# Kernel optimization log

Hardware: AMD Instinct MI355X
Metric: run time of the kernel (lower is better)

## Reference

```python
import jax, jax.numpy as jnp
import numpy as np

B, S, H, L, NH, OUT = 64, 512, 512, 2, 8, 1
HD = H // NH
SKIP_INTERVAL = 2
EPS = 1e-5


def ln(x, g, b):
    m = x.mean(-1, keepdims=True)
    v = x.var(-1, keepdims=True)
    return (x - m) / jnp.sqrt(v + EPS) * g + b


def setup_inputs() -> dict:
    key = jax.random.key(0)
    ks = iter(jax.random.split(key, 64))
    def nrm(shape, s=0.02):
        return jax.random.normal(next(ks), shape, jnp.float32) * s
    inp = {
        'x': jax.random.normal(next(ks), (B, S, H), jnp.float32),
        # stacked per-layer LSTM params (input_size == hidden_size == H)
        'Wi': nrm((L, 4 * H, H)), 'bi': jnp.zeros((L, 4 * H), jnp.float32).at[:, H:2 * H].set(1.0),
        'Wh': nrm((L, 4 * H, H)), 'bh': jnp.zeros((L, 4 * H), jnp.float32).at[:, H:2 * H].set(1.0),
        'g_in': jnp.ones((L, 4 * H), jnp.float32), 'b_in': jnp.zeros((L, 4 * H), jnp.float32),
        'g_hid': jnp.ones((L, 4 * H), jnp.float32), 'b_hid': jnp.zeros((L, 4 * H), jnp.float32),
        'g_cell': jnp.ones((L, H), jnp.float32), 'b_cell': jnp.zeros((L, H), jnp.float32),
        # highway per layer
        'hw_Wt': nrm((L, H, H)), 'hw_bt': jnp.zeros((L, H), jnp.float32),
        'hw_Wc': nrm((L, H, H)), 'hw_bc': jnp.full((L, H), -1.0, jnp.float32),
        'hw_Wh': nrm((L, H, H)), 'hw_bh': jnp.zeros((L, H), jnp.float32),
        # attention
        'Wq': nrm((H, H)), 'bq': jnp.zeros((H,), jnp.float32),
        'Wk': nrm((H, H)), 'bk': jnp.zeros((H,), jnp.float32),
        'Wv': nrm((H, H)), 'bv': jnp.zeros((H,), jnp.float32),
        'Wo': nrm((H, H)), 'bo': jnp.zeros((H,), jnp.float32),
        'att_g': jnp.ones((H,), jnp.float32), 'att_b': jnp.zeros((H,), jnp.float32),
        # output norm + projection head
        'on_g': jnp.ones((H,), jnp.float32), 'on_b': jnp.zeros((H,), jnp.float32),
        'Wp1': nrm((H // 2, H)), 'bp1': jnp.zeros((H // 2,), jnp.float32),
        'Wp2': nrm((OUT, H // 2)), 'bp2': jnp.zeros((OUT,), jnp.float32),
    }
    return inp


def _forward(x, Wi, bi, Wh, bh, g_in, b_in, g_hid, b_hid, g_cell, b_cell,
             hw_Wt, hw_bt, hw_Wc, hw_bc, hw_Wh, hw_bh,
             Wq, bq, Wk, bk, Wv, bv, Wo, bo, att_g, att_b,
             on_g, on_b, Wp1, bp1, Wp2, bp2):
    def lstm_layer(seq, l):
        # precompute input projection + its LayerNorm for all timesteps: [B,S,4H]
        ip = ln(jnp.einsum('bsh,gh->bsg', seq, Wi[l]) + bi[l], g_in[l], b_in[l])
        def step(carry, ip_t):
            h, c = carry
            hp = ln(h @ Wh[l].T + bh[l], g_hid[l], b_hid[l])
            i_, f_, g_, o_ = jnp.split(ip_t + hp, 4, axis=-1)
            c = jax.nn.sigmoid(f_) * c + jax.nn.sigmoid(i_) * jnp.tanh(g_)
            h = jax.nn.sigmoid(o_) * jnp.tanh(ln(c, g_cell[l], b_cell[l]))
            return (h, c), h
        h0 = jnp.zeros((seq.shape[0], H), seq.dtype)
        _, hs = jax.lax.scan(step, (h0, h0), jnp.swapaxes(ip, 0, 1))
        return jnp.swapaxes(hs, 0, 1)  # [B,S,H]

    seq = x
    for l in range(L):
        h_seq = lstm_layer(seq, l)
        # highway network
        tg = jax.nn.sigmoid(h_seq @ hw_Wt[l].T + hw_bt[l])
        cg = jax.nn.sigmoid(h_seq @ hw_Wc[l].T + hw_bc[l])
        tr = jax.nn.relu(h_seq @ hw_Wh[l].T + hw_bh[l])
        h_seq = tg * tr + cg * h_seq
        # skip connection every SKIP_INTERVAL layers
        if l > 0 and (l + 1) % SKIP_INTERVAL == 0:
            h_seq = h_seq + seq
        seq = h_seq

    # multi-head self-attention with residual + LayerNorm
    def heads(y):
        return jnp.swapaxes(y.reshape(B, S, NH, HD), 1, 2)  # [B,NH,S,HD]
    q = heads(seq @ Wq.T + bq)
    k = heads(seq @ Wk.T + bk)
    v = heads(seq @ Wv.T + bv)
    scale = 1.0 / float(np.sqrt(HD))
    scores = jnp.einsum('bnqd,bnkd->bnqk', q, k) * scale
    aw = jax.nn.softmax(scores, axis=-1)
    ctx = jnp.einsum('bnqk,bnkd->bnqd', aw, v)
    ctx = jnp.swapaxes(ctx, 1, 2).reshape(B, S, H)
    att = ln(ctx @ Wo.T + bo + seq, att_g, att_b)

    # last timestep -> output norm -> MLP head
    last = ln(att[:, -1], on_g, on_b)
    hmid = jax.nn.relu(last @ Wp1.T + bp1)
    return hmid @ Wp2.T + bp2  # [B, OUT]


def reference(x, Wi, bi, Wh, bh, g_in, b_in, g_hid, b_hid, g_cell, b_cell,
              hw_Wt, hw_bt, hw_Wc, hw_bc, hw_Wh, hw_bh,
              Wq, bq, Wk, bk, Wv, bv, Wo, bo, att_g, att_b,
              on_g, on_b, Wp1, bp1, Wp2, bp2):
    return _forward(x, Wi, bi, Wh, bh, g_in, b_in, g_hid, b_hid, g_cell, b_cell,
                    hw_Wt, hw_bt, hw_Wc, hw_bc, hw_Wh, hw_bh,
                    Wq, bq, Wk, bk, Wv, bv, Wo, bo, att_g, att_b,
                    on_g, on_b, Wp1, bp1, Wp2, bp2)
```

## Files before the change

### kernel.cpp

```cpp
#include <hip/hip_runtime.h>

#define EPS_LN 1e-5f

static constexpr int Bn  = 64;
static constexpr int Sn  = 512;
static constexpr int Hn  = 512;
static constexpr int G4n = 2048;

typedef unsigned int uint32;
typedef unsigned long long uint64;
typedef _Float16 h2v __attribute__((ext_vector_type(2)));

__device__ __forceinline__ float sigf(float x)     { return 1.0f / (1.0f + __expf(-x)); }
__device__ __forceinline__ float tanhfast(float x) { return 1.0f - 2.0f / (1.0f + __expf(2.0f * x)); }

__device__ __forceinline__ float dot2h(uint32 w, uint32 h, float acc) {
#if defined(__has_builtin)
#if __has_builtin(__builtin_amdgcn_fdot2)
  return __builtin_amdgcn_fdot2(__builtin_bit_cast(h2v, w), __builtin_bit_cast(h2v, h), acc, false);
#define DOT2_DONE 1
#endif
#endif
#ifndef DOT2_DONE
  h2v wv = __builtin_bit_cast(h2v, w);
  h2v hv = __builtin_bit_cast(h2v, h);
  return acc + (float)wv.x * (float)hv.x + (float)wv.y * (float)hv.y;
#endif
}
__device__ __forceinline__ uint32 packh2(float a, float b) {
  h2v v; v.x = (_Float16)a; v.y = (_Float16)b;
  return __builtin_bit_cast(uint32, v);
}

__device__ __forceinline__ float blk_sum(float v, float* sm, int tid) {
#pragma unroll
  for (int o = 32; o; o >>= 1) v += __shfl_down(v, o, 64);
  __syncthreads();
  if ((tid & 63) == 0) sm[tid >> 6] = v;
  __syncthreads();
  return sm[0] + sm[1] + sm[2] + sm[3];
}
__device__ __forceinline__ float blk_max(float v, float* sm, int tid) {
#pragma unroll
  for (int o = 32; o; o >>= 1) v = fmaxf(v, __shfl_down(v, o, 64));
  __syncthreads();
  if ((tid & 63) == 0) sm[tid >> 6] = v;
  __syncthreads();
  return fmaxf(fmaxf(sm[0], sm[1]), fmaxf(sm[2], sm[3]));
}

__device__ __forceinline__ void blk_sum4_w8(float& a, float& b, float& c, float& d,
                                            float* sm, int tid) {
#pragma unroll
  for (int o = 32; o; o >>= 1) {
    a += __shfl_down(a, o, 64);
    b += __shfl_down(b, o, 64);
    c += __shfl_down(c, o, 64);
    d += __shfl_down(d, o, 64);
  }
  __syncthreads();
  if ((tid & 63) == 0) {
    float4 v; v.x = a; v.y = b; v.z = c; v.w = d;
    *(float4*)&sm[(tid >> 6) * 4] = v;
  }
  __syncthreads();
  float ra = 0.f, rb = 0.f, rc = 0.f, rd = 0.f;
#pragma unroll
  for (int w = 0; w < 8; ++w) {
    float4 v = *(const float4*)&sm[w * 4];
    ra += v.x; rb += v.y; rc += v.z; rd += v.w;
  }
  a = ra; b = rb; c = rc; d = rd;
}

__global__ __launch_bounds__(256) void wh_pack_k(
    const float* __restrict__ Wh, uint32* __restrict__ WhP)
{
  __shared__ float tile[32][33];
  const int l = blockIdx.z;
  const int k0 = blockIdx.x * 32;
  const int n0 = blockIdx.y * 32;
  const int row = threadIdx.x >> 5, col = threadIdx.x & 31;
  const float* src = Wh + (long)l * G4n * Hn;
  uint32* dst = WhP + (long)l * 256 * G4n;
#pragma unroll
  for (int rr = 0; rr < 4; ++rr) {
    int nn = row + rr * 8;
    tile[nn][col] = src[(long)(n0 + nn) * Hn + k0 + col];
  }
  __syncthreads();
#pragma unroll
  for (int rr = 0; rr < 2; ++rr) {
    int kpl = row + rr * 8;
    int kp = (k0 >> 1) + kpl;
    dst[(long)kp * G4n + n0 + col] = packh2(tile[col][2*kpl], tile[col][2*kpl+1]);
  }
}

__global__ void init_zbuf_k(uint64* zbuf)
{
  long i = (long)blockIdx.x * 512 + threadIdx.x;
  zbuf[i] = 0ULL;
}

__global__ __launch_bounds__(256) void gemm_ip_k(
    const float* __restrict__ A,
    const float* __restrict__ Bw,
    const float* __restrict__ bias,
    uint32* __restrict__ C,
    int s0)
{
  __shared__ __align__(16) uint32 Ah[8][128];
  __shared__ __align__(16) uint32 Bh[8][128];
  const int tid = threadIdx.x;
  const long m0 = (long)blockIdx.y * 128;
  const long n0 = (long)blockIdx.x * 128;
  const int tx = tid & 15, ty = tid >> 4;
  const int lrow = tid >> 1;
  const int lc0  = (tid & 1) * 8;
  const int kb   = (tid & 1) * 4;
  float acc[8][8];
#pragma unroll
  for (int i = 0; i < 8; ++i)
#pragma unroll
    for (int j = 0; j < 8; ++j) acc[i][j] = 0.f;

  const long r  = m0 + lrow;
  const long b  = r & 63;
  const long sl = r >> 6;
  const float* Arow = A + (b * Sn + s0 + sl) * Hn;
  const float* Brow = Bw + (n0 + lrow) * 512L;

  float4 a0 = *(const float4*)(Arow + lc0);
  float4 a1 = *(const float4*)(Arow + lc0 + 4);
  float4 b0 = *(const float4*)(Brow + lc0);
  float4 b1 = *(const float4*)(Brow + lc0 + 4);

  for (int k0 = 0; k0 < 512; k0 += 16) {
    __syncthreads();
    Ah[kb+0][lrow] = packh2(a0.x, a0.y);
    Ah[kb+1][lrow] = packh2(a0.z, a0.w);
    Ah[kb+2][lrow] = packh2(a1.x, a1.y);
    Ah[kb+3][lrow] = packh2(a1.z, a1.w);
    Bh[kb+0][lrow] = packh2(b0.x, b0.y);
    Bh[kb+1][lrow] = packh2(b0.z, b0.w);
    Bh[kb+2][lrow] = packh2(b1.x, b1.y);
    Bh[kb+3][lrow] = packh2(b1.z, b1.w);
    __syncthreads();
    if (k0 + 16 < 512) {
      a0 = *(const float4*)(Arow + k0 + 16 + lc0);
      a1 = *(const float4*)(Arow + k0 + 16 + lc0 + 4);
      b0 = *(const float4*)(Brow + k0 + 16 + lc0);
      b1 = *(const float4*)(Brow + k0 + 16 + lc0 + 4);
    }
#pragma unroll
    for (int kp = 0; kp < 8; ++kp) {
      uint32 a8[8], b8[8];
      *(uint4*)&a8[0] = *(const uint4*)&Ah[kp][ty*8];
      *(uint4*)&a8[4] = *(const uint4*)&Ah[kp][ty*8+4];
      *(uint4*)&b8[0] = *(const uint4*)&Bh[kp][tx*8];
      *(uint4*)&b8[4] = *(const uint4*)&Bh[kp][tx*8+4];
#pragma unroll
      for (int i = 0; i < 8; ++i)
#pragma unroll
        for (int j = 0; j < 8; ++j) acc[i][j] = dot2h(a8[i], b8[j], acc[i][j]);
    }
  }
#pragma unroll
  for (int i = 0; i < 8; ++i) {
    long m = m0 + ty*8 + i;
    uint32* crow = C + m * 1024 + (n0 >> 1) + tx*4;
    const float* br = bias + n0 + tx*8;
    uint4 o;
    o.x = packh2(acc[i][0]+br[0], acc[i][1]+br[1]);
    o.y = packh2(acc[i][2]+br[2], acc[i][3]+br[3]);
    o.z = packh2(acc[i][4]+br[4], acc[i][5]+br[5]);
    o.w = packh2(acc[i][6]+br[6], acc[i][7]+br[7]);
    *(uint4*)crow = o;
  }
}

__global__ __launch_bounds__(256) void ipstats_k(
    const uint32* __restrict__ X, float* __restrict__ st)
{
  const long row = blockIdx.x;
  const uint32* xr = X + row * 1024;
  const int tid = threadIdx.x;
  __shared__ float sm[4];
  uint4 w = *(const uint4*)(xr + tid*4);
  h2v a = __builtin_bit_cast(h2v, w.x);
  h2v b = __builtin_bit_cast(h2v, w.y);
  h2v c = __builtin_bit_cast(h2v, w.z);
  h2v d = __builtin_bit_cast(h2v, w.w);
  float v[8] = {(float)a.x,(float)a.y,(float)b.x,(float)b.y,
                (float)c.x,(float)c.y,(float)d.x,(float)d.y};
  float s1 = 0.f, s2 = 0.f;
#pragma unroll
  for (int i = 0; i < 8; ++i) { s1 += v[i]; s2 += v[i]*v[i]; }
  s1 = blk_sum(s1, sm, tid);
  s2 = blk_sum(s2, sm, tid);
  if (tid == 0) {
    const float mean = s1 * (1.f/2048.f);
    const float rstd = rsqrtf(s2 * (1.f/2048.f) - mean*mean + EPS_LN);
    st[row*2]     = mean;
    st[row*2 + 1] = rstd;
  }
}

__global__ __launch_bounds__(256) void hw_fused_k(
    const float* __restrict__ A,
    const float* __restrict__ Wt, const float* __restrict__ bt,
    const float* __restrict__ Wc, const float* __restrict__ bc,
    const float* __restrict__ Wh3, const float* __restrict__ bh3,
    float* __restrict__ seqout,
    int skip)
{
  __shared__ __align__(16) uint32 Ah[8][128];
  __shared__ __align__(16) uint32 Bh[3][8][68];
  const int tid = threadIdx.x;
  const long m0 = (long)blockIdx.y * 128;
  const int n0 = blockIdx.x * 64;
  const int tx = tid & 7;
  const int ty = tid >> 3;
  const int lrow = tid >> 1;
  const int lc0  = (tid & 1) * 8;
  const int kbA  = (tid & 1) * 4;
  const int brow = tid >> 2;
  const int bk0  = (tid & 3) * 4;
  const int kbB  = (tid & 3) * 2;

  float accT[4][8], accC[4][8], accH[4][8];
#pragma unroll
  for (int i = 0; i < 4; ++i)
#pragma unroll
    for (int j = 0; j < 8; ++j) { accT[i][j] = 0.f; accC[i][j] = 0.f; accH[i][j] = 0.f; }

  const float* Arow = A + (m0 + lrow) * 512;
  const long boff = (long)(n0 + brow) * 512 + bk0;

  float4 a0 = *(const float4*)(Arow + lc0);
  float4 a1 = *(const float4*)(Arow + lc0 + 4);
  float4 wt4 = *(const float4*)(Wt  + boff);
  float4 wc4 = *(const float4*)(Wc  + boff);
  float4 wh4 = *(const float4*)(Wh3 + boff);

  for (int k0 = 0; k0 < 512; k0 += 16) {
    __syncthreads();
    Ah[kbA+0][lrow] = packh2(a0.x, a0.y);
    Ah[kbA+1][lrow] = packh2(a0.z, a0.w);
    Ah[kbA+2][lrow] = packh2(a1.x, a1.y);
    Ah[kbA+3][lrow] = packh2(a1.z, a1.w);
    Bh[0][kbB+0][brow] = packh2(wt4.x, wt4.y);
    Bh[0][kbB+1][brow] = packh2(wt4.z, wt4.w);
    Bh[1][kbB+0][brow] = packh2(wc4.x, wc4.y);
    Bh[1][kbB+1][brow] = packh2(wc4.z, wc4.w);
    Bh[2][kbB+0][brow] = packh2(wh4.x, wh4.y);
    Bh[2][kbB+1][brow] = packh2(wh4.z, wh4.w);
    __syncthreads();
    if (k0 + 16 < 512) {
      a0 = *(const float4*)(Arow + k0 + 16 + lc0);
      a1 = *(const float4*)(Arow + k0 + 16 + lc0 + 4);
      wt4 = *(const float4*)(Wt  + boff + k0 + 16);
      wc4 = *(const float4*)(Wc  + boff + k0 + 16);
      wh4 = *(const float4*)(Wh3 + boff + k0 + 16);
    }
#pragma unroll
    for (int kp = 0; kp < 8; ++kp) {
      uint32 a4[4];
      *(uint4*)&a4[0] = *(const uint4*)&Ah[kp][ty*4];
      {
        uint32 b8[8];
        *(uint4*)&b8[0] = *(const uint4*)&Bh[0][kp][tx*8];
        *(uint4*)&b8[4] = *(const uint4*)&Bh[0][kp][tx*8+4];
#pragma unroll
        for (int i = 0; i < 4; ++i)
#pragma unroll
          for (int j = 0; j < 8; ++j) accT[i][j] = dot2h(a4[i], b8[j], accT[i][j]);
      }
      {
        uint32 b8[8];
        *(uint4*)&b8[0] = *(const uint4*)&Bh[1][kp][tx*8];
        *(uint4*)&b8[4] = *(const uint4*)&Bh[1][kp][tx*8+4];
#pragma unroll
        for (int i = 0; i < 4; ++i)
#pragma unroll
          for (int j = 0; j < 8; ++j) accC[i][j] = dot2h(a4[i], b8[j], accC[i][j]);
      }
      {
        uint32 b8[8];
        *(uint4*)&b8[0] = *(const uint4*)&Bh[2][kp][tx*8];
        *(uint4*)&b8[4] = *(const uint4*)&Bh[2][kp][tx*8+4];
#pragma unroll
        for (int i = 0; i < 4; ++i)
#pragma unroll
          for (int j = 0; j < 8; ++j) accH[i][j] = dot2h(a4[i], b8[j], accH[i][j]);
      }
    }
  }

  float btr[8], bcr[8], bhr[8];
#pragma unroll
  for (int j = 0; j < 8; ++j) {
    btr[j] = bt[n0 + tx*8 + j];
    bcr[j] = bc[n0 + tx*8 + j];
    bhr[j] = bh3[n0 + tx*8 + j];
  }
#pragma unroll
  for (int i = 0; i < 4; ++i) {
    const long m = m0 + ty*4 + i;
    const float* hrow = A + m * 512 + n0 + tx*8;
    float* srow = seqout + m * 512 + n0 + tx*8;
    float4 h0 = *(const float4*)hrow;
    float4 h1 = *(const float4*)(hrow + 4);
    float hv[8] = {h0.x,h0.y,h0.z,h0.w,h1.x,h1.y,h1.z,h1.w};
    float sv[8] = {0,0,0,0,0,0,0,0};
    if (skip) {
      float4 s0 = *(const float4*)srow;
      float4 s1 = *(const float4*)(srow + 4);
      sv[0]=s0.x; sv[1]=s0.y; sv[2]=s0.z; sv[3]=s0.w;
      sv[4]=s1.x; sv[5]=s1.y; sv[6]=s1.z; sv[7]=s1.w;
    }
    float o[8];
#pragma unroll
    for (int j = 0; j < 8; ++j) {
      const float t1 = accT[i][j] + btr[j];
      const float t2 = accC[i][j] + bcr[j];
      const float t3 = accH[i][j] + bhr[j];
      o[j] = sigf(t1) * fmaxf(t3, 0.f) + sigf(t2) * hv[j] + sv[j];
    }
    float4 o0, o1;
    o0.x=o[0]; o0.y=o[1]; o0.z=o[2]; o0.w=o[3];
    o1.x=o[4]; o1.y=o[5]; o1.z=o[6]; o1.w=o[7];
    *(float4*)srow = o0; *(float4*)(srow + 4) = o1;
  }
}

__global__ __launch_bounds__(256) void gemm_m64_k(
    const float* __restrict__ A, long lda,
    const float* __restrict__ Bw,
    const float* __restrict__ bias,
    float* __restrict__ P,
    int N, int K)
{
  __shared__ float As[64][64];
  __shared__ float Bs[64][64];
  const int tid = threadIdx.x;
  const int n0 = blockIdx.x * 64;
  const int kc = blockIdx.y;
  const int Kc = K / gridDim.y;
  const int tx = tid & 15, ty = tid >> 4;
  const int row = tid >> 2, q = tid & 3;
  float acc[4][4];
#pragma unroll
  for (int i = 0; i < 4; ++i)
#pragma unroll
    for (int j = 0; j < 4; ++j) acc[i][j] = 0.f;

  for (int k0 = kc * Kc; k0 < kc * Kc + Kc; k0 += 64) {
    float4 a[4], b[4];
#pragma unroll
    for (int c = 0; c < 4; ++c) {
      a[c] = *(const float4*)(A  + (long)row * lda       + k0 + q*16 + c*4);
      b[c] = *(const float4*)(Bw + (long)(n0 + row) * K  + k0 + q*16 + c*4);
    }
    __syncthreads();
#pragma unroll
    for (int c = 0; c < 4; ++c) {
      int kb = q*16 + c*4;
      As[kb+0][row]=a[c].x; As[kb+1][row]=a[c].y; As[kb+2][row]=a[c].z; As[kb+3][row]=a[c].w;
      Bs[kb+0][row]=b[c].x; Bs[kb+1][row]=b[c].y; Bs[kb+2][row]=b[c].z; Bs[kb+3][row]=b[c].w;
    }
    __syncthreads();
#pragma unroll
    for (int kk = 0; kk < 64; ++kk) {
      float4 av = *(const float4*)&As[kk][ty*4];
      float4 bv = *(const float4*)&Bs[kk][tx*4];
      float am[4] = {av.x, av.y, av.z, av.w};
      float bm[4] = {bv.x, bv.y, bv.z, bv.w};
#pragma unroll
      for (int i = 0; i < 4; ++i)
#pragma unroll
        for (int j = 0; j < 4; ++j) acc[i][j] += am[i] * bm[j];
    }
  }
#pragma unroll
  for (int i = 0; i < 4; ++i) {
    int m = ty*4 + i;
    float* pr = P + ((long)kc * 64 + m) * N + n0 + tx*4;
#pragma unroll
    for (int j = 0; j < 4; ++j) {
      float bb = bias ? bias[n0 + tx*4 + j] : 0.f;
      pr[j] = acc[i][j] + bb;
    }
  }
}

__global__ __launch_bounds__(512, 2) void lstm_seqz_k(
    const uint32* __restrict__ WhP,
    const float* __restrict__ bh,
    const uint32* __restrict__ ipc,
    const float* __restrict__ ipstats,
    const float* __restrict__ g_in, const float* __restrict__ b_in,
    const float* __restrict__ g_hid, const float* __restrict__ b_hid,
    const float* __restrict__ g_cell, const float* __restrict__ b_cell,
    float* __restrict__ hst, float* __restrict__ cst,
    float* __restrict__ hseq,
    uint64* __restrict__ zbuf,
    int t0, int nsteps, int gbase)
{
  const int blk = blockIdx.x;
  const int g   = blk & 31;
  const int kq  = blk >> 5;
  const int tid = threadIdx.x;
  const int b0  = g*2, b1 = g*2 + 1;
  const int r   = tid >> 1;
  const int kh  = tid & 1;
  __shared__ __align__(16) uint32 hp0[264];
  __shared__ __align__(16) uint32 hp1[264];
  __shared__ float sm[32];

  uint4 wreg[32];
  {
    const uint32* base = WhP + (long)(kh * 128) * 2048 + (kq*256 + r);
#pragma unroll
    for (int i = 0; i < 32; ++i) {
      wreg[i].x = base[(long)(4*i + 0) * 2048];
      wreg[i].y = base[(long)(4*i + 1) * 2048];
      wreg[i].z = base[(long)(4*i + 2) * 2048];
      wreg[i].w = base[(long)(4*i + 3) * 2048];
    }
  }

  float bhr[4], ghr[4], bhir[4], ginr[4], binr[4];
#pragma unroll
  for (int q = 0; q < 4; ++q) {
    bhr[q]  = bh[q*512 + tid];
    ghr[q]  = g_hid[q*512 + tid];
    bhir[q] = b_hid[q*512 + tid];
    ginr[q] = g_in[q*512 + tid];
    binr[q] = b_in[q*512 + tid];
  }
  const float gcv = g_cell[tid];
  const float bcv = b_cell[tid];
  float c0 = cst[b0*512 + tid];
  float c1 = cst[b1*512 + tid];
  float h0 = hst[b0*512 + tid];
  float h1 = hst[b1*512 + tid];

  {
    const float p0 = __shfl_xor(h0, 1, 64);
    const float p1 = __shfl_xor(h1, 1, 64);
    if (!(tid & 1)) {
      const int j = tid >> 1;
      const int jj = (j < 128) ? j : j + 4;
      hp0[jj] = packh2(h0, p0);
      hp1[jj] = packh2(h1, p1);
    }
  }
  __syncthreads();

  const long myword = (long)(kq*256 + r) * 2 + kh;
  const uint32* hb0 = hp0 + kh * 132;
  const uint32* hb1 = hp1 + kh * 132;

  for (int ts = 0; ts < nsteps; ++ts) {
    const int gstep = gbase + ts;
    const uint32 tagw = (uint32)gstep;
    uint64* zp = zbuf + (long)(gstep & 1) * 131072 + (long)g * 4096;

    const uint32* iprow0 = ipc + ((long)ts * 64 + b0) * 1024 + (tid >> 1);
    const uint32* iprow1 = ipc + ((long)ts * 64 + b1) * 1024 + (tid >> 1);
    const float2 st0 = *(const float2*)(ipstats + ((long)ts * 64 + b0) * 2);
    const float2 st1 = *(const float2*)(ipstats + ((long)ts * 64 + b1) * 2);
    float ip0[4], ip1[4];
#pragma unroll
    for (int q = 0; q < 4; ++q) {
      h2v v0 = __builtin_bit_cast(h2v, iprow0[q*256]);
      h2v v1 = __builtin_bit_cast(h2v, iprow1[q*256]);
      const float r0 = kh ? (float)v0.y : (float)v0.x;
      const float r1 = kh ? (float)v1.y : (float)v1.x;
      ip0[q] = (r0 - st0.x) * st0.y * ginr[q] + binr[q];
      ip1[q] = (r1 - st1.x) * st1.y * ginr[q] + binr[q];
    }

    float a0 = 0.f, a1 = 0.f;
#pragma unroll
    for (int i = 0; i < 32; ++i) {
      const uint4 w  = wreg[i];
      const uint4 hv0 = *(const uint4*)&hb0[4*i];
      const uint4 hv1 = *(const uint4*)&hb1[4*i];
      a0 = dot2h(w.x, hv0.x, a0); a0 = dot2h(w.y, hv0.y, a0);
      a0 = dot2h(w.z, hv0.z, a0); a0 = dot2h(w.w, hv0.w, a0);
      a1 = dot2h(w.x, hv1.x, a1); a1 = dot2h(w.y, hv1.y, a1);
      a1 = dot2h(w.z, hv1.z, a1); a1 = dot2h(w.w, hv1.w, a1);
    }
    a0 += __shfl_xor(a0, 1, 64);
    a1 += __shfl_xor(a1, 1, 64);

    {
      const float zval = kh ? a1 : a0;
      const uint64 w = ((uint64)tagw << 32) | (uint64)__builtin_bit_cast(uint32, zval);
      __hip_atomic_store(zp + myword, w, __ATOMIC_RELAXED, __HIP_MEMORY_SCOPE_AGENT);
    }

    float z0[4], z1[4];
    {
      uint64 v0[4], v1[4];
      int pend = 0xff;
      while (pend) {
#pragma unroll
        for (int q = 0; q < 4; ++q) {
          const long base = (long)(q*512 + tid) * 2;
          if (pend & (1 << q)) {
            uint64 w = __hip_atomic_load(zp + base, __ATOMIC_RELAXED, __HIP_MEMORY_SCOPE_AGENT);
            if ((uint32)(w >> 32) == tagw) { v0[q] = w; pend &= ~(1 << q); }
          }
          if (pend & (16 << q)) {
            uint64 w = __hip_atomic_load(zp + base + 1, __ATOMIC_RELAXED, __HIP_MEMORY_SCOPE_AGENT);
            if ((uint32)(w >> 32) == tagw) { v1[q] = w; pend &= ~(16 << q); }
          }
        }
        if (pend) __builtin_amdgcn_s_sleep(2);
      }
#pragma unroll
      for (int q = 0; q < 4; ++q) {
        z0[q] = __builtin_bit_cast(float, (uint32)v0[q]) + bhr[q];
        z1[q] = __builtin_bit_cast(float, (uint32)v1[q]) + bhr[q];
      }
    }

    float s10 = z0[0]+z0[1]+z0[2]+z0[3];
    float s20 = z0[0]*z0[0] + z0[1]*z0[1] + z0[2]*z0[2] + z0[3]*z0[3];
    float s11 = z1[0]+z1[1]+z1[2]+z1[3];
    float s21 = z1[0]*z1[0] + z1[1]*z1[1] + z1[2]*z1[2] + z1[3]*z1[3];
    blk_sum4_w8(s10, s20, s11, s21, sm, tid);
    const float m0 = s10 * (1.f/2048.f);
    const float r0 = rsqrtf(s20 * (1.f/2048.f) - m0*m0 + EPS_LN);
    const float m1 = s11 * (1.f/2048.f);
    const float r1 = rsqrtf(s21 * (1.f/2048.f) - m1*m1 + EPS_LN);

    const float gi0 = ip0[0] + (z0[0] - m0) * r0 * ghr[0] + bhir[0];
    const float gf0 = ip0[1] + (z0[1] - m0) * r0 * ghr[1] + bhir[1];
    const float gg0 = ip0[2] + (z0[2] - m0) * r0 * ghr[2] + bhir[2];
    const float go0 = ip0[3] + (z0[3] - m0) * r0 * ghr[3] + bhir[3];
    const float gi1 = ip1[0] + (z1[0] - m1) * r1 * ghr[0] + bhir[0];
    const float gf1 = ip1[1] + (z1[1] - m1) * r1 * ghr[1] + bhir[1];
    const float gg1 = ip1[2] + (z1[2] - m1) * r1 * ghr[2] + bhir[2];
    const float go1 = ip1[3] + (z1[3] - m1) * r1 * ghr[3] + bhir[3];

    c0 = sigf(gf0) * c0 + sigf(gi0) * tanhfast(gg0);
    c1 = sigf(gf1) * c1 + sigf(gi1) * tanhfast(gg1);

    float t10 = c0, t20 = c0*c0, t11 = c1, t21 = c1*c1;
    blk_sum4_w8(t10, t20, t11, t21, sm, tid);
    const float n0 = t10 * (1.f/512.f);
    const float q0r = rsqrtf(t20 * (1.f/512.f) - n0*n0 + EPS_LN);
    const float n1 = t11 * (1.f/512.f);
    const float q1r = rsqrtf(t21 * (1.f/512.f) - n1*n1 + EPS_LN);
    h0 = sigf(go0) * tanhfast((c0 - n0) * q0r * gcv + bcv);
    h1 = sigf(go1) * tanhfast((c1 - n1) * q1r * gcv + bcv);

    if (kq == 0) {
      hseq[((long)b0 * Sn + t0 + ts) * Hn + tid] = h0;
      hseq[((long)b1 * Sn + t0 + ts) * Hn + tid] = h1;
    }

    const float p0 = __shfl_xor(h0, 1, 64);
    const float p1 = __shfl_xor(h1, 1, 64);
    if (!(tid & 1)) {
      const int j = tid >> 1;
      const int jj = (j < 128) ? j : j + 4;
      hp0[jj] = packh2(h0, p0);
      hp1[jj] = packh2(h1, p1);
    }
    __syncthreads();
  }
  if (kq == 0) {
    hst[b0*512 + tid] = h0; hst[b1*512 + tid] = h1;
    cst[b0*512 + tid] = c0; cst[b1*512 + tid] = c1;
  }
}

__global__ void init_hc_k(float* h, float* c)
{
  int i = blockIdx.x * 256 + threadIdx.x;
  h[i] = 0.f; c[i] = 0.f;
}

__global__ __launch_bounds__(256) void qkh_k(
    const float* __restrict__ qlst, const float* __restrict__ Wk,
    const float* __restrict__ bk,
    float* __restrict__ qkh, float* __restrict__ qbk)
{
  const int hd = blockIdx.x, cg = blockIdx.y;
  const int b = threadIdx.x & 63, sc = threadIdx.x >> 6;
  const int col0 = cg * 128 + sc * 32;
  float qreg[64];
  const float* qp = qlst + b*512 + hd*64;
#pragma unroll
  for (int j4 = 0; j4 < 16; ++j4) {
    float4 v = *(const float4*)(qp + j4*4);
    qreg[j4*4+0]=v.x; qreg[j4*4+1]=v.y; qreg[j4*4+2]=v.z; qreg[j4*4+3]=v.w;
  }
  float acc[32];
#pragma unroll
  for (int c = 0; c < 32; ++c) acc[c] = 0.f;
  for (int j = 0; j < 64; ++j) {
    float qv = qreg[j];
    const float* wr = Wk + (long)(hd*64 + j)*512 + col0;
#pragma unroll
    for (int c4 = 0; c4 < 8; ++c4) {
      float4 w = *(const float4*)(wr + c4*4);
      acc[c4*4+0] = __builtin_fmaf(qv, w.x, acc[c4*4+0]);
      acc[c4*4+1] = __builtin_fmaf(qv, w.y, acc[c4*4+1]);
      acc[c4*4+2] = __builtin_fmaf(qv, w.z, acc[c4*4+2]);
      acc[c4*4+3] = __builtin_fmaf(qv, w.w, acc[c4*4+3]);
    }
  }
  float* op = qkh + ((long)b*8 + hd)*512 + col0;
#pragma unroll
  for (int c4 = 0; c4 < 8; ++c4) {
    float4 o;
    o.x = acc[c4*4+0]; o.y = acc[c4*4+1]; o.z = acc[c4*4+2]; o.w = acc[c4*4+3];
    *(float4*)(op + c4*4) = o;
  }
  if (cg == 0 && sc == 0) {
    float s = 0.f;
    for (int j = 0; j < 64; ++j) s += qreg[j] * bk[hd*64 + j];
    qbk[b*8 + hd] = s;
  }
}

__global__ __launch_bounds__(256) void attn2_k(
    const float* __restrict__ seq,
    const float* __restrict__ qkh,
    const float* __restrict__ qbk,
    float* __restrict__ u)
{
  const int b = blockIdx.x, hd = blockIdx.y, tid = threadIdx.x;
  __shared__ __align__(16) float qk[512];
  __shared__ float p[512];
  __shared__ float sm[4];
  qk[tid]       = qkh[((long)b*8 + hd)*512 + tid];
  qk[tid + 256] = qkh[((long)b*8 + hd)*512 + tid + 256];
  __syncthreads();
  const float bias = qbk[b*8 + hd];

  float loc[2]; float mx = -3.0e38f;
#pragma unroll
  for (int v = 0; v < 2; ++v) {
    int s = tid + v*256;
    const float4* sr = (const float4*)(seq + ((long)b*512 + s)*512);
    const float4* qv4 = (const float4*)qk;
    float d = 0.f;
    for (int k4 = 0; k4 < 128; ++k4) {
      float4 sv = sr[k4], qv = qv4[k4];
      d += sv.x*qv.x + sv.y*qv.y + sv.z*qv.z + sv.w*qv.w;
    }
    d = (d + bias) * 0.125f;
    loc[v] = d; mx = fmaxf(mx, d);
  }
  const float M = blk_max(mx, sm, tid);
  float sum = 0.f;
#pragma unroll
  for (int v = 0; v < 2; ++v) {
    int s = tid + v*256;
    float e = __expf(loc[v] - M);
    p[s] = e; sum += e;
  }
  const float SM = blk_sum(sum, sm, tid);
  const float inv = 1.f / SM;

  float u0 = 0.f, u1 = 0.f;
  for (int s = 0; s < 512; ++s) {
    float ps = p[s];
    const float* srow = seq + ((long)b*512 + s)*512;
    u0 = __builtin_fmaf(ps, srow[tid], u0);
    u1 = __builtin_fmaf(ps, srow[tid + 256], u1);
  }
  u[((long)b*8 + hd)*512 + tid]       = u0 * inv;
  u[((long)b*8 + hd)*512 + tid + 256] = u1 * inv;
}

__global__ __launch_bounds__(256) void ctxv_k(
    const float* __restrict__ u, const float* __restrict__ Wv,
    const float* __restrict__ bv, float* __restrict__ ctx)
{
  const int b = blockIdx.x, tid = threadIdx.x;
  __shared__ __align__(16) float ul[8*512];
  for (int i = tid; i < 4096; i += 256) ul[i] = u[(long)b*4096 + i];
  __syncthreads();
#pragma unroll
  for (int v = 0; v < 2; ++v) {
    int n = tid + v*256;
    int hd = n >> 6;
    const float4* wr = (const float4*)(Wv + (long)n*512);
    const float4* uv = (const float4*)&ul[hd*512];
    float acc = 0.f;
    for (int k4 = 0; k4 < 128; ++k4) {
      float4 w = wr[k4], x = uv[k4];
      acc += w.x*x.x + w.y*x.y + w.z*x.z + w.w*x.w;
    }
    ctx[b*512 + n] = acc + bv[n];
  }
}

__global__ __launch_bounds__(256) void head_k(
    const float* __restrict__ ctx,
    const float* __restrict__ Wo, const float* __restrict__ bo,
    const float* __restrict__ seq,
    const float* __restrict__ att_g, const float* __restrict__ att_b,
    const float* __restrict__ on_g, const float* __restrict__ on_b,
    const float* __restrict__ Wp1, const float* __restrict__ bp1,
    const float* __restrict__ Wp2, const float* __restrict__ bp2,
    float* __restrict__ out)
{
  const int b = blockIdx.x, tid = threadIdx.x;
  __shared__ __align__(16) float cs[512];
  __shared__ __align__(16) float buf[512];
  __shared__ float sm[4];
  cs[tid]       = ctx[b*512 + tid];
  cs[tid + 256] = ctx[b*512 + tid + 256];
  __syncthreads();

  const float* srow = seq + ((long)b*512 + 511) * 512;
  float o[2];
#pragma unroll
  for (int v = 0; v < 2; ++v) {
    int j = tid + v*256;
    const float4* w4 = (const float4*)(Wo + (long)j * 512);
    const float4* c4 = (const float4*)cs;
    float acc = 0.f;
    for (int kx = 0; kx < 128; ++kx) {
      float4 w = w4[kx], c = c4[kx];
      acc += w.x*c.x + w.y*c.y + w.z*c.z + w.w*c.w;
    }
    o[v] = acc + bo[j] + srow[j];
  }
  float s1 = o[0] + o[1], s2 = o[0]*o[0] + o[1]*o[1];
  s1 = blk_sum(s1, sm, tid); s2 = blk_sum(s2, sm, tid);
  float m1 = s1 * (1.f/512.f);
  float r1 = rsqrtf(s2 * (1.f/512.f) - m1*m1 + EPS_LN);
  float a[2];
#pragma unroll
  for (int v = 0; v < 2; ++v) {
    int j = tid + v*256;
    a[v] = (o[v] - m1) * r1 * att_g[j] + att_b[j];
  }
  s1 = a[0] + a[1]; s2 = a[0]*a[0] + a[1]*a[1];
  s1 = blk_sum(s1, sm, tid); s2 = blk_sum(s2, sm, tid);
  float m2 = s1 * (1.f/512.f);
  float r2 = rsqrtf(s2 * (1.f/512.f) - m2*m2 + EPS_LN);
#pragma unroll
  for (int v = 0; v < 2; ++v) {
    int j = tid + v*256;
    buf[j] = (a[v] - m2) * r2 * on_g[j] + on_b[j];
  }
  __syncthreads();

  const float4* w1 = (const float4*)(Wp1 + (long)tid * 512);
  const float4* b4 = (const float4*)buf;
  float acc = 0.f;
  for (int kx = 0; kx < 128; ++kx) {
    float4 w = w1[kx], c = b4[kx];
    acc += w.x*c.x + w.y*c.y + w.z*c.z + w.w*c.w;
  }
  float mid = fmaxf(acc + bp1[tid], 0.f);
  float contrib = mid * Wp2[tid];
  float tot = blk_sum(contrib, sm, tid);
  if (tid == 0) out[b] = tot + bp2[0];
}

extern "C" void kernel_launch(void* const* d_in, const int* in_sizes, int n_in,
                              void* d_out, int out_size, void* d_ws, size_t ws_size,
                              hipStream_t stream)
{
  const float* x     = (const float*)d_in[0];
  const float* Wi    = (const float*)d_in[1];
  const float* bi    = (const float*)d_in[2];
  const float* Wh    = (const float*)d_in[3];
  const float* bh    = (const float*)d_in[4];
  const float* g_in  = (const float*)d_in[5];
  const float* b_in  = (const float*)d_in[6];
  const float* g_hid = (const float*)d_in[7];
  const float* b_hid = (const float*)d_in[8];
  const float* g_cell= (const float*)d_in[9];
  const float* b_cell= (const float*)d_in[10];
  const float* hwWt  = (const float*)d_in[11];
  const float* hwbt  = (const float*)d_in[12];
  const float* hwWc  = (const float*)d_in[13];
  const float* hwbc  = (const float*)d_in[14];
  const float* hwWh  = (const float*)d_in[15];
  const float* hwbh  = (const float*)d_in[16];
  const float* Wq    = (const float*)d_in[17];
  const float* bq    = (const float*)d_in[18];
  const float* Wk    = (const float*)d_in[19];
  const float* bk    = (const float*)d_in[20];
  const float* Wv    = (const float*)d_in[21];
  const float* bv    = (const float*)d_in[22];
  const float* Wo    = (const float*)d_in[23];
  const float* bo    = (const float*)d_in[24];
  const float* att_g = (const float*)d_in[25];
  const float* att_b = (const float*)d_in[26];
  const float* on_g  = (const float*)d_in[27];
  const float* on_b  = (const float*)d_in[28];
  const float* Wp1   = (const float*)d_in[29];
  const float* bp1   = (const float*)d_in[30];
  const float* Wp2   = (const float*)d_in[31];
  const float* bp2   = (const float*)d_in[32];
  float* out = (float*)d_out;

  const long SEQF = (long)Bn * Sn * Hn;
  const long WHPF = 2L * 256 * G4n;
  const long ZBF  = 2L * 32 * 2048 * 2;
  const long wsF  = (long)(ws_size / 4);

  float* ws   = (float*)d_ws;
  float* seq  = ws;
  float* hseq = seq  + SEQF;
  uint32* WhP = (uint32*)(hseq + SEQF);
  uint64* zbuf = (uint64*)(hseq + SEQF + WHPF);
  float* hst  = hseq + SEQF + WHPF + 2*ZBF;
  float* cst  = hst  + 32768L;
  float* qlst = cst  + 32768L;
  float* ctx  = qlst + 32768L;
  float* qkh  = ctx  + 32768L;
  float* qbk  = qkh  + 262144L;
  float* uat  = qbk  + 1024L;
  float* ipstats = uat + 262144L;
  float* ipcF = ipstats + 32768L;
  uint32* ipc = (uint32*)ipcF;
  const long baseF = (ipcF - ws);

  int TCH = 256;
  while (TCH > 16 && baseF + (long)TCH * 64 * 1024 > wsF) TCH >>= 1;

  wh_pack_k<<<dim3(16, 64, 2), 256, 0, stream>>>(Wh, WhP);
  init_zbuf_k<<<512, 512, 0, stream>>>(zbuf);

  const int NCH = Sn / TCH;
  const int MROWS = TCH * 64;
  const int NMCH = (Bn * Sn) / MROWS;

  for (int l = 0; l < 2; ++l) {
    const float* seqin = (l == 0) ? x : seq;
    init_hc_k<<<128, 256, 0, stream>>>(hst, cst);
    for (int c = 0; c < NCH; ++c) {
      const int s0 = c * TCH;
      gemm_ip_k<<<dim3(16, TCH/2), 256, 0, stream>>>(seqin, Wi + (long)l*G4n*Hn, bi + l*G4n, ipc, s0);
      ipstats_k<<<TCH*64, 256, 0, stream>>>(ipc, ipstats);
      lstm_seqz_k<<<256, 512, 0, stream>>>(WhP + (long)l*256*G4n, bh + l*G4n, ipc, ipstats,
          g_in + l*G4n, b_in + l*G4n,
          g_hid + l*G4n, b_hid + l*G4n, g_cell + l*Hn, b_cell + l*Hn,
          hst, cst, hseq, zbuf, s0, TCH, l*Sn + s0 + 1);
    }
    for (int mc = 0; mc < NMCH; ++mc) {
      const long m0 = (long)mc * MROWS;
      hw_fused_k<<<dim3(8, MROWS/128), 256, 0, stream>>>(
          hseq + m0*512,
          hwWt + (long)l*Hn*Hn, hwbt + l*Hn,
          hwWc + (long)l*Hn*Hn, hwbc + l*Hn,
          hwWh + (long)l*Hn*Hn, hwbh + l*Hn,
          seq + m0*512, (l == 0) ? 0 : 1);
    }
  }

  gemm_m64_k<<<dim3(8, 1), 256, 0, stream>>>(seq + 511L*512, 512L*512, Wq, bq, qlst, 512, 512);
  qkh_k<<<dim3(8, 4), 256, 0, stream>>>(qlst, Wk, bk, qkh, qbk);
  attn2_k<<<dim3(64, 8), 256, 0, stream>>>(seq, qkh, qbk, uat);
  ctxv_k<<<64, 256, 0, stream>>>(uat, Wv, bv, ctx);
  head_k<<<64, 256, 0, stream>>>(ctx, Wo, bo, seq, att_g, att_b, on_g, on_b, Wp1, bp1, Wp2, bp2, out);
}
```

Measured before the change: 9.067 ms.

## Use MFMA f16 instructions for LSTM input-projection GEMM and enlarge time chunk

Replaces the scalar fdot2-based register-tiled GEMM for the LSTM input projection with MFMA 16x16x32 f16 matrix instructions. Shared memory is restructured into a padded row-major staging layout and the K step widens to 32. The chunk size TCH doubles to 512 so the projection for a whole layer runs in one launch, and the ipstats region is enlarged. The larger chunk needs more workspace, and the epilogue stores through a lane shuffle with scattered 32-bit writes.

```diff
diff --git a/kernel.cpp b/kernel.cpp
--- a/kernel.cpp
+++ b/kernel.cpp
@@ -10,6 +10,8 @@
 typedef unsigned int uint32;
 typedef unsigned long long uint64;
 typedef _Float16 h2v __attribute__((ext_vector_type(2)));
+typedef _Float16 h8v __attribute__((ext_vector_type(8)));
+typedef float f4v __attribute__((ext_vector_type(4)));
 
 __device__ __forceinline__ float sigf(float x)     { return 1.0f / (1.0f + __expf(-x)); }
 __device__ __forceinline__ float tanhfast(float x) { return 1.0f - 2.0f / (1.0f + __expf(2.0f * x)); }
@@ -110,73 +112,105 @@
     uint32* __restrict__ C,
     int s0)
 {
-  __shared__ __align__(16) uint32 Ah[8][128];
-  __shared__ __align__(16) uint32 Bh[8][128];
+  __shared__ __align__(16) uint32 Ast[128 * 20];
+  __shared__ __align__(16) uint32 Bst[128 * 20];
   const int tid = threadIdx.x;
   const long m0 = (long)blockIdx.y * 128;
-  const long n0 = (long)blockIdx.x * 128;
-  const int tx = tid & 15, ty = tid >> 4;
-  const int lrow = tid >> 1;
-  const int lc0  = (tid & 1) * 8;
-  const int kb   = (tid & 1) * 4;
-  float acc[8][8];
-#pragma unroll
-  for (int i = 0; i < 8; ++i)
-#pragma unroll
-    for (int j = 0; j < 8; ++j) acc[i][j] = 0.f;
-
-  const long r  = m0 + lrow;
+  const int n0 = blockIdx.x * 128;
+
+  const int rt = tid >> 1;
+  const int hf = tid & 1;
+  const long r  = m0 + rt;
   const long b  = r & 63;
   const long sl = r >> 6;
-  const float* Arow = A + (b * Sn + s0 + sl) * Hn;
-  const float* Brow = Bw + (n0 + lrow) * 512L;
-
-  float4 a0 = *(const float4*)(Arow + lc0);
-  float4 a1 = *(const float4*)(Arow + lc0 + 4);
-  float4 b0 = *(const float4*)(Brow + lc0);
-  float4 b1 = *(const float4*)(Brow + lc0 + 4);
-
-  for (int k0 = 0; k0 < 512; k0 += 16) {
+  const float* Arow = A + (b * Sn + s0 + sl) * Hn + hf * 16;
+  const float* Brow = Bw + (long)(n0 + rt) * 512 + hf * 16;
+  const int sbase = rt * 20 + hf * 8;
+
+  const int w  = tid >> 6;
+  const int l  = tid & 63;
+  const int lr = l & 15;
+  const int lk = (l >> 4) * 4;
+
+  f4v acc[8][2];
+#pragma unroll
+  for (int ct = 0; ct < 8; ++ct)
+#pragma unroll
+    for (int mt = 0; mt < 2; ++mt) {
+      acc[ct][mt][0] = 0.f; acc[ct][mt][1] = 0.f;
+      acc[ct][mt][2] = 0.f; acc[ct][mt][3] = 0.f;
+    }
+
+  float4 pa0 = *(const float4*)(Arow + 0);
+  float4 pa1 = *(const float4*)(Arow + 4);
+  float4 pa2 = *(const float4*)(Arow + 8);
+  float4 pa3 = *(const float4*)(Arow + 12);
+  float4 pb0 = *(const float4*)(Brow + 0);
+  float4 pb1 = *(const float4*)(Brow + 4);
+  float4 pb2 = *(const float4*)(Brow + 8);
+  float4 pb3 = *(const float4*)(Brow + 12);
+
+  for (int ks = 0; ks < 16; ++ks) {
     __syncthreads();
-    Ah[kb+0][lrow] = packh2(a0.x, a0.y);
-    Ah[kb+1][lrow] = packh2(a0.z, a0.w);
-    Ah[kb+2][lrow] = packh2(a1.x, a1.y);
-    Ah[kb+3][lrow] = packh2(a1.z, a1.w);
-    Bh[kb+0][lrow] = packh2(b0.x, b0.y);
-    Bh[kb+1][lrow] = packh2(b0.z, b0.w);
-    Bh[kb+2][lrow] = packh2(b1.x, b1.y);
-    Bh[kb+3][lrow] = packh2(b1.z, b1.w);
+    {
+      uint4 ua0, ua1, ub0, ub1;
+      ua0.x = packh2(pa0.x, pa0.y); ua0.y = packh2(pa0.z, pa0.w);
+      ua0.z = packh2(pa1.x, pa1.y); ua0.w = packh2(pa1.z, pa1.w);
+      ua1.x = packh2(pa2.x, pa2.y); ua1.y = packh2(pa2.z, pa2.w);
+      ua1.z = packh2(pa3.x, pa3.y); ua1.w = packh2(pa3.z, pa3.w);
+      ub0.x = packh2(pb0.x, pb0.y); ub0.y = packh2(pb0.z, pb0.w);
+      ub0.z = packh2(pb1.x, pb1.y); ub0.w = packh2(pb1.z, pb1.w);
+      ub1.x = packh2(pb2.x, pb2.y); ub1.y = packh2(pb2.z, pb2.w);
+      ub1.z = packh2(pb3.x, pb3.y); ub1.w = packh2(pb3.z, pb3.w);
+      *(uint4*)&Ast[sbase]     = ua0;
+      *(uint4*)&Ast[sbase + 4] = ua1;
+      *(uint4*)&Bst[sbase]     = ub0;
+      *(uint4*)&Bst[sbase + 4] = ub1;
+    }
     __syncthreads();
-    if (k0 + 16 < 512) {
-      a0 = *(const float4*)(Arow + k0 + 16 + lc0);
-      a1 = *(const float4*)(Arow + k0 + 16 + lc0 + 4);
-      b0 = *(const float4*)(Brow + k0 + 16 + lc0);
-      b1 = *(const float4*)(Brow + k0 + 16 + lc0 + 4);
-    }
-#pragma unroll
-    for (int kp = 0; kp < 8; ++kp) {
-      uint32 a8[8], b8[8];
-      *(uint4*)&a8[0] = *(const uint4*)&Ah[kp][ty*8];
-      *(uint4*)&a8[4] = *(const uint4*)&Ah[kp][ty*8+4];
-      *(uint4*)&b8[0] = *(const uint4*)&Bh[kp][tx*8];
-      *(uint4*)&b8[4] = *(const uint4*)&Bh[kp][tx*8+4];
-#pragma unroll
-      for (int i = 0; i < 8; ++i)
-#pragma unroll
-        for (int j = 0; j < 8; ++j) acc[i][j] = dot2h(a8[i], b8[j], acc[i][j]);
-    }
-  }
-#pragma unroll
-  for (int i = 0; i < 8; ++i) {
-    long m = m0 + ty*8 + i;
-    uint32* crow = C + m * 1024 + (n0 >> 1) + tx*4;
-    const float* br = bias + n0 + tx*8;
-    uint4 o;
-    o.x = packh2(acc[i][0]+br[0], acc[i][1]+br[1]);
-    o.y = packh2(acc[i][2]+br[2], acc[i][3]+br[3]);
-    o.z = packh2(acc[i][4]+br[4], acc[i][5]+br[5]);
-    o.w = packh2(acc[i][6]+br[6], acc[i][7]+br[7]);
-    *(uint4*)crow = o;
+    if (ks + 1 < 16) {
+      const int ko = (ks + 1) * 32;
+      pa0 = *(const float4*)(Arow + ko + 0);
+      pa1 = *(const float4*)(Arow + ko + 4);
+      pa2 = *(const float4*)(Arow + ko + 8);
+      pa3 = *(const float4*)(Arow + ko + 12);
+      pb0 = *(const float4*)(Brow + ko + 0);
+      pb1 = *(const float4*)(Brow + ko + 4);
+      pb2 = *(const float4*)(Brow + ko + 8);
+      pb3 = *(const float4*)(Brow + ko + 12);
+    }
+    uint4 aw0 = *(const uint4*)&Ast[(w*32 + lr) * 20 + lk];
+    uint4 aw1 = *(const uint4*)&Ast[(w*32 + 16 + lr) * 20 + lk];
+    h8v af0 = __builtin_bit_cast(h8v, aw0);
+    h8v af1 = __builtin_bit_cast(h8v, aw1);
+#pragma unroll
+    for (int ct = 0; ct < 8; ++ct) {
+      uint4 bw4 = *(const uint4*)&Bst[(ct*16 + lr) * 20 + lk];
+      h8v bf = __builtin_bit_cast(h8v, bw4);
+      acc[ct][0] = __builtin_amdgcn_mfma_f32_16x16x32_f16(af0, bf, acc[ct][0], 0, 0, 0);
+      acc[ct][1] = __builtin_amdgcn_mfma_f32_16x16x32_f16(af1, bf, acc[ct][1], 0, 0, 0);
+    }
+  }
+
+  float bs[8];
+#pragma unroll
+  for (int ct = 0; ct < 8; ++ct) bs[ct] = bias[n0 + ct*16 + lr];
+  const long mbase = m0 + w*32 + (l >> 4) * 4;
+#pragma unroll
+  for (int ct = 0; ct < 8; ++ct) {
+    const int cp = (n0 + ct*16 + lr) >> 1;
+#pragma unroll
+    for (int mt = 0; mt < 2; ++mt) {
+#pragma unroll
+      for (int j = 0; j < 4; ++j) {
+        float v = acc[ct][mt][j] + bs[ct];
+        float vh = __shfl_xor(v, 1, 64);
+        if (!(l & 1)) {
+          const long m = mbase + mt*16 + j;
+          C[m * 1024 + cp] = packh2(v, vh);
+        }
+      }
+    }
   }
 }
 
@@ -828,11 +862,11 @@
   float* qbk  = qkh  + 262144L;
   float* uat  = qbk  + 1024L;
   float* ipstats = uat + 262144L;
-  float* ipcF = ipstats + 32768L;
+  float* ipcF = ipstats + 65536L;
   uint32* ipc = (uint32*)ipcF;
   const long baseF = (ipcF - ws);
 
-  int TCH = 256;
+  int TCH = 512;
   while (TCH > 16 && baseF + (long)TCH * 64 * 1024 > wsF) TCH >>= 1;
 
   wh_pack_k<<<dim3(16, 64, 2), 256, 0, stream>>>(Wh, WhP);
```

New measurement: 8.463 ms. -6.7%, faster.
